# Performance work log

Measured on AMD Instinct MI355X. Metric: run time of the kernel, lower is better.

## Reference

```python
import jax, jax.numpy as jnp
import numpy as np
from jax import lax

HID, PROJ, DYN = 256, 256, 64
HW, BS, NQ = 6400, 16, 100


def setup_inputs() -> dict:
    key = jax.random.key(0)
    ks = jax.random.split(key, 10)
    p = lambda k, shape: jax.random.normal(k, shape, jnp.float32) * 0.02
    return {
        "query_feat": jax.random.normal(ks[0], (HW, BS, HID), jnp.float32),
        "support_feat": jax.random.normal(ks[1], (NQ, BS, HID), jnp.float32),
        "h": 80,
        "w": 80,
        "Wq": p(ks[2], (HID, PROJ)), "bq": jnp.zeros((PROJ,), jnp.float32),
        "Ws": p(ks[3], (HID, PROJ)), "bsp": jnp.zeros((PROJ,), jnp.float32),
        "W1": p(ks[4], (PROJ, DYN)), "b1": jnp.zeros((DYN,), jnp.float32),
        "W2": p(ks[5], (DYN, HID)), "b2": jnp.zeros((HID,), jnp.float32),
    }


def reference(query_feat, support_feat, h, w, Wq, bq, Ws, bsp, W1, b1, W2, b2):
    # query_feat: [hw, bs, c] -> [bs, hw, c]; support_feat: [nq, bs, c] -> [bs, nq, c]
    qf = jnp.transpose(query_feat, (1, 0, 2))
    sf = jnp.transpose(support_feat, (1, 0, 2))
    bsz, nq = sf.shape[0], sf.shape[1]
    hw = h * w

    fs_proj = sf @ Ws + bsp                      # [bs, nq, proj]
    fq_proj = qf @ Wq + bq                       # [bs, hw, proj]
    pattern = jnp.tanh(jax.nn.relu(fs_proj @ W1 + b1) @ W2 + b2)
    fs_feat = (pattern + 1.0) * fs_proj          # [bs, nq, proj]

    # bmm(fq, fs^T).T -> [bs, nq, hw]
    sim = jnp.einsum("bkp,bnp->bnk", fq_proj, fs_feat)
    similarity = sim.reshape(bsz, nq, h, w)

    # coordinate grid: x varies along w, y along h; flattened [hw, 2]
    gy = jnp.arange(h, dtype=jnp.float32) + 0.5
    gx = jnp.arange(w, dtype=jnp.float32) + 0.5
    X, Y = jnp.meshgrid(gx, gy, indexing="xy")  # each [h, w]
    coord = jnp.stack([X, Y], axis=-1).reshape(hw, 2)
    side = jnp.array([w, h], dtype=jnp.float32)

    sm = jax.nn.softmax(sim, axis=-1)            # [bs, nq, hw]
    proposal_for_loss = jnp.einsum("bnk,kd->bnd", sm, coord) / side

    # argmax peak -> one-hot -> 3x3 max-pool dilation (note (w,h) reshape per original)
    max_pos = jnp.argmax(sim, axis=-1)           # [bs, nq]
    max_mask = jax.nn.one_hot(max_pos, hw, dtype=jnp.float32).reshape(bsz, nq, w, h)
    local_mask = lax.reduce_window(
        max_mask, -jnp.inf, lax.max,
        window_dimensions=(1, 1, 3, 3), window_strides=(1, 1, 1, 1),
        padding=[(0, 0), (0, 0), (1, 1), (1, 1)],
    ).reshape(bsz, nq, hw)

    local_sm = sm * local_mask
    local_sm = local_sm / (jnp.sum(local_sm, axis=-1, keepdims=True) + 1e-10)
    proposals = jnp.einsum("bnk,kd->bnd", local_sm, coord) / side

    return proposal_for_loss, similarity, proposals
```

## Files before the change

### kernel.cpp

```cpp
#include <hip/hip_runtime.h>

#define HID 256
#define PROJ 256
#define DYN 64
#define HWD 6400
#define BSZ 16
#define NQ 100
#define HH 80
#define WW 80

typedef unsigned short u16;
typedef u16 u16x8 __attribute__((ext_vector_type(8)));
typedef __bf16 bf16x8 __attribute__((ext_vector_type(8)));
typedef float f32x4 __attribute__((ext_vector_type(4)));

__device__ __forceinline__ float bf2f(u16 h) {
    union { unsigned u; float f; } c; c.u = ((unsigned)h) << 16; return c.f;
}
__device__ __forceinline__ u16 f2bf(float f) {
    union { float f; unsigned u; } c; c.f = f;
    return (u16)((c.u + 0x7FFFu + ((c.u >> 16) & 1u)) >> 16);
}

__global__ __launch_bounds__(1024, 1) void kpre(
    const float* __restrict__ support,
    const float* __restrict__ Wq, const float* __restrict__ bq,
    const float* __restrict__ Ws, const float* __restrict__ bsp,
    const float* __restrict__ W1, const float* __restrict__ b1,
    const float* __restrict__ W2, const float* __restrict__ b2,
    u16* __restrict__ pack, float* __restrict__ cvec)
{
    const int c = blockIdx.x;
    const int b = blockIdx.y;
    const int t = threadIdx.x;

    __shared__ __align__(16) float sf_t[HID][8];
    __shared__ __align__(16) float part[4][8][256];
    __shared__ __align__(16) float fsp[8][PROJ];
    __shared__ __align__(16) float hidp[2][8][DYN];
    __shared__ __align__(16) float hid[8][DYN];
    __shared__ __align__(16) float fsf_t[PROJ][8];
    __shared__ float cacc[8][4];

    const int g = t >> 8;
    const int p = t & 255;

    {
        const int nl = t >> 7;
        const int i0 = (t & 127) * 2;
        const int n = c * 8 + nl;
        float v0 = 0.f, v1 = 0.f;
        if (n < NQ) {
            const float* sp = support + (size_t)n * (BSZ * HID) + (size_t)b * HID + i0;
            const float2 a = *reinterpret_cast<const float2*>(sp);
            v0 = a.x; v1 = a.y;
        }
        sf_t[i0][nl] = v0;
        sf_t[i0 + 1][nl] = v1;
    }
    __syncthreads();

    {
        float acc[8];
        #pragma unroll
        for (int n = 0; n < 8; ++n) acc[n] = 0.f;
        const int ibase = g * 64;
        float w[64];
        #pragma unroll
        for (int j = 0; j < 64; ++j)
            w[j] = Ws[(size_t)(ibase + j) * PROJ + p];
        __builtin_amdgcn_sched_barrier(0);
        #pragma unroll
        for (int j = 0; j < 64; ++j) {
            const f32x4 s0 = *reinterpret_cast<const f32x4*>(&sf_t[ibase + j][0]);
            const f32x4 s1 = *reinterpret_cast<const f32x4*>(&sf_t[ibase + j][4]);
            acc[0] += s0[0] * w[j]; acc[1] += s0[1] * w[j];
            acc[2] += s0[2] * w[j]; acc[3] += s0[3] * w[j];
            acc[4] += s1[0] * w[j]; acc[5] += s1[1] * w[j];
            acc[6] += s1[2] * w[j]; acc[7] += s1[3] * w[j];
        }
        #pragma unroll
        for (int n = 0; n < 8; ++n) part[g][n][p] = acc[n];
    }
    __syncthreads();
    {
        const int na = t >> 8;
        const float bb = bsp[p];
        #pragma unroll
        for (int k = 0; k < 2; ++k) {
            const int n = na + k * 4;
            fsp[n][p] = part[0][n][p] + part[1][n][p] + part[2][n][p] + part[3][n][p] + bb;
        }
    }
    __syncthreads();

    {
        const int ph = t >> 9;
        const int n = (t >> 6) & 7;
        const int d = t & 63;
        float a = 0.f;
        const int pb0 = ph * 128;
        #pragma unroll
        for (int pb = 0; pb < 128; pb += 64) {
            float w[64];
            #pragma unroll
            for (int j = 0; j < 64; ++j)
                w[j] = W1[(size_t)(pb0 + pb + j) * DYN + d];
            __builtin_amdgcn_sched_barrier(0);
            #pragma unroll
            for (int j = 0; j < 64; j += 4) {
                const f32x4 s = *reinterpret_cast<const f32x4*>(&fsp[n][pb0 + pb + j]);
                a += s[0] * w[j] + s[1] * w[j + 1] + s[2] * w[j + 2] + s[3] * w[j + 3];
            }
        }
        hidp[ph][n][d] = a;
    }
    __syncthreads();
    if (t < 512) {
        const int n = t >> 6, d = t & 63;
        const float a = hidp[0][n][d] + hidp[1][n][d] + b1[d];
        hid[n][d] = a > 0.f ? a : 0.f;
    }
    __syncthreads();

    {
        const int nh = t >> 8;
        const int n0 = nh * 2, n1 = nh * 2 + 1;
        const float bqv = bq[p];
        const float b2v = b2[p];
        float w[64];
        #pragma unroll
        for (int d = 0; d < 64; ++d) w[d] = W2[(size_t)d * PROJ + p];
        __builtin_amdgcn_sched_barrier(0);
        float a0 = 0.f, a1 = 0.f;
        #pragma unroll
        for (int d0 = 0; d0 < 64; d0 += 4) {
            const f32x4 h0 = *reinterpret_cast<const f32x4*>(&hid[n0][d0]);
            const f32x4 h1 = *reinterpret_cast<const f32x4*>(&hid[n1][d0]);
            a0 += h0[0] * w[d0] + h0[1] * w[d0 + 1] + h0[2] * w[d0 + 2] + h0[3] * w[d0 + 3];
            a1 += h1[0] * w[d0] + h1[1] * w[d0 + 1] + h1[2] * w[d0 + 2] + h1[3] * w[d0 + 3];
        }
        const float pat0 = tanhf(a0 + b2v);
        const float pat1 = tanhf(a1 + b2v);
        const float ff0 = (pat0 + 1.f) * fsp[n0][p];
        const float ff1 = (pat1 + 1.f) * fsp[n1][p];
        *reinterpret_cast<float2*>(&fsf_t[p][n0]) = make_float2(ff0, ff1);
        float cp0 = bqv * ff0, cp1 = bqv * ff1;
        for (int off = 32; off > 0; off >>= 1) {
            cp0 += __shfl_down(cp0, off);
            cp1 += __shfl_down(cp1, off);
        }
        const int lane = t & 63;
        const int ps = (t >> 6) & 3;
        if (lane == 0) { cacc[n0][ps] = cp0; cacc[n1][ps] = cp1; }
    }
    __syncthreads();
    if (t < 8) {
        const int n = c * 8 + t;
        if (n < NQ) cvec[b * NQ + n] = cacc[t][0] + cacc[t][1] + cacc[t][2] + cacc[t][3];
    }

    {
        const int h = p;
        float acc[8];
        #pragma unroll
        for (int n = 0; n < 8; ++n) acc[n] = 0.f;
        const int pbase = g * 64;
        f32x4 wv4[16];
        #pragma unroll
        for (int k = 0; k < 16; ++k)
            wv4[k] = *reinterpret_cast<const f32x4*>(Wq + (size_t)h * PROJ + pbase + k * 4);
        __builtin_amdgcn_sched_barrier(0);
        #pragma unroll
        for (int k = 0; k < 16; ++k) {
            #pragma unroll
            for (int m = 0; m < 4; ++m) {
                const int pp = pbase + k * 4 + m;
                const float w = wv4[k][m];
                const f32x4 f0 = *reinterpret_cast<const f32x4*>(&fsf_t[pp][0]);
                const f32x4 f1 = *reinterpret_cast<const f32x4*>(&fsf_t[pp][4]);
                acc[0] += f0[0] * w; acc[1] += f0[1] * w;
                acc[2] += f0[2] * w; acc[3] += f0[3] * w;
                acc[4] += f1[0] * w; acc[5] += f1[1] * w;
                acc[6] += f1[2] * w; acc[7] += f1[3] * w;
            }
        }
        #pragma unroll
        for (int n = 0; n < 8; ++n) part[g][n][h] = acc[n];
    }
    __syncthreads();

    {
        const int h = p;
        const int na = t >> 8;
        const int ks = h >> 5, quad = (h >> 3) & 3, j = h & 7;
        const int nt = c >> 1;
        #pragma unroll
        for (int k = 0; k < 2; ++k) {
            const int nl = na + k * 4;
            const int n = c * 8 + nl;
            float f = part[0][nl][h] + part[1][nl][h] + part[2][nl][h] + part[3][nl][h];
            if (n >= NQ) f = 0.f;
            const u16 hi = f2bf(f);
            const u16 lo = f2bf(f - bf2f(hi));
            const int nit = (c & 1) * 8 + nl;
            const int lane2 = quad * 16 + nit;
            const size_t base = ((((size_t)b * 2 + 0) * 8 + ks) * 8 + nt) * 512 + lane2 * 8 + j;
            pack[base] = hi;
            pack[base + (size_t)8 * 8 * 512] = lo;
        }
    }
}

__global__ __launch_bounds__(256, 3) void ksim(
    const float* __restrict__ qf,
    const u16* __restrict__ pack,
    const float* __restrict__ cvec,
    float* __restrict__ sim)
{
    const int mc = blockIdx.x;
    const int b  = blockIdx.y;
    const int wv = threadIdx.x >> 6;
    const int lane = threadIdx.x & 63;
    const int quad = lane >> 4, l16 = lane & 15;

    __shared__ __align__(16) u16 sbuf[2][14][512];

    const u16* pbase = pack + (size_t)b * (2 * 8 * 8 * 64 * 8);

    #define STAGE(KS, BUF)                                                          \
        do {                                                                        \
            for (int s14 = wv; s14 < 14; s14 += 4) {                                \
                const int s_ = s14 / 7, nt_ = s14 % 7;                              \
                const u16* g_ = pbase + ((size_t)(s_ * 8 + (KS)) * 8 + nt_) * 512   \
                                + (size_t)lane * 8;                                 \
                __builtin_amdgcn_global_load_lds(                                   \
                    (const __attribute__((address_space(1))) void*)g_,              \
                    (__attribute__((address_space(3))) void*)&sbuf[BUF][s14][0],    \
                    16, 0, 0);                                                      \
            }                                                                       \
        } while (0)

    f32x4 acc[7];
    #pragma unroll
    for (int nt = 0; nt < 7; ++nt) acc[nt] = (f32x4){0.f, 0.f, 0.f, 0.f};

    const int row = mc * 64 + wv * 16 + l16;
    const float* ap = qf + (size_t)row * (BSZ * HID) + b * HID + quad * 8;

    f32x4 af[16];
    {
        const float* p0 = ap + 0 * 32;
        const float* p1 = ap + 1 * 32;
        const float* p2 = ap + 2 * 32;
        const float* p3 = ap + 3 * 32;
        const float* p4 = ap + 4 * 32;
        const float* p5 = ap + 5 * 32;
        const float* p6 = ap + 6 * 32;
        const float* p7 = ap + 7 * 32;
        asm volatile(
            "global_load_dwordx4 %0, %16, off\n\t"
            "global_load_dwordx4 %1, %16, off offset:16\n\t"
            "global_load_dwordx4 %2, %17, off\n\t"
            "global_load_dwordx4 %3, %17, off offset:16\n\t"
            "global_load_dwordx4 %4, %18, off\n\t"
            "global_load_dwordx4 %5, %18, off offset:16\n\t"
            "global_load_dwordx4 %6, %19, off\n\t"
            "global_load_dwordx4 %7, %19, off offset:16\n\t"
            "global_load_dwordx4 %8, %20, off\n\t"
            "global_load_dwordx4 %9, %20, off offset:16\n\t"
            "global_load_dwordx4 %10, %21, off\n\t"
            "global_load_dwordx4 %11, %21, off offset:16\n\t"
            "global_load_dwordx4 %12, %22, off\n\t"
            "global_load_dwordx4 %13, %22, off offset:16\n\t"
            "global_load_dwordx4 %14, %23, off\n\t"
            "global_load_dwordx4 %15, %23, off offset:16\n\t"
            "s_waitcnt vmcnt(0)"
            : "=&v"(af[0]), "=&v"(af[1]), "=&v"(af[2]), "=&v"(af[3]),
              "=&v"(af[4]), "=&v"(af[5]), "=&v"(af[6]), "=&v"(af[7]),
              "=&v"(af[8]), "=&v"(af[9]), "=&v"(af[10]), "=&v"(af[11]),
              "=&v"(af[12]), "=&v"(af[13]), "=&v"(af[14]), "=&v"(af[15])
            : "v"(p0), "v"(p1), "v"(p2), "v"(p3),
              "v"(p4), "v"(p5), "v"(p6), "v"(p7));
    }

    STAGE(0, 0);

    bf16x8 Ahi[8], Alo[8];
    #pragma unroll
    for (int ks = 0; ks < 8; ++ks) {
        #pragma unroll
        for (int j = 0; j < 4; ++j) {
            const float v0 = af[2 * ks][j];
            const __bf16 h0 = (__bf16)v0;
            Ahi[ks][j] = h0; Alo[ks][j] = (__bf16)(v0 - (float)h0);
            const float v1 = af[2 * ks + 1][j];
            const __bf16 h1 = (__bf16)v1;
            Ahi[ks][4 + j] = h1; Alo[ks][4 + j] = (__bf16)(v1 - (float)h1);
        }
    }
    __syncthreads();

    int buf = 0;
    #pragma unroll
    for (int ks = 0; ks < 8; ++ks) {
        if (ks < 7) STAGE(ks + 1, buf ^ 1);

        u16x8 uh[7];
        #pragma unroll
        for (int nt = 0; nt < 7; ++nt)
            uh[nt] = *reinterpret_cast<const u16x8*>(&sbuf[buf][nt][lane * 8]);
        #pragma unroll
        for (int nt = 0; nt < 7; ++nt) {
            const bf16x8 bh = __builtin_bit_cast(bf16x8, uh[nt]);
            acc[nt] = __builtin_amdgcn_mfma_f32_16x16x32_bf16(Ahi[ks], bh, acc[nt], 0, 0, 0);
        }
        #pragma unroll
        for (int nt = 0; nt < 7; ++nt) {
            const bf16x8 bh = __builtin_bit_cast(bf16x8, uh[nt]);
            acc[nt] = __builtin_amdgcn_mfma_f32_16x16x32_bf16(Alo[ks], bh, acc[nt], 0, 0, 0);
        }

        u16x8 ul[7];
        #pragma unroll
        for (int nt = 0; nt < 7; ++nt)
            ul[nt] = *reinterpret_cast<const u16x8*>(&sbuf[buf][7 + nt][lane * 8]);
        #pragma unroll
        for (int nt = 0; nt < 7; ++nt) {
            const bf16x8 bl = __builtin_bit_cast(bf16x8, ul[nt]);
            acc[nt] = __builtin_amdgcn_mfma_f32_16x16x32_bf16(Ahi[ks], bl, acc[nt], 0, 0, 0);
        }

        __syncthreads();
        buf ^= 1;
    }
    #undef STAGE

    const int kbase = mc * 64 + wv * 16 + quad * 4;
    #pragma unroll
    for (int nt = 0; nt < 7; ++nt) {
        const int n = nt * 16 + l16;
        if (n >= NQ) continue;
        const float cadd = cvec[b * NQ + n];
        f32x4 o = acc[nt];
        o[0] += cadd; o[1] += cadd; o[2] += cadd; o[3] += cadd;
        *reinterpret_cast<f32x4*>(sim + (size_t)(b * NQ + n) * HWD + kbase) = o;
    }
}

__global__ __launch_bounds__(128, 2) void kfin(
    const float* __restrict__ sim,
    float* __restrict__ out)
{
    const int bn = blockIdx.x;
    const int w = threadIdx.x >> 6;
    const int lane = threadIdx.x & 63;
    const float* src = sim + (size_t)bn * HWD;

    __shared__ float redf[2][8];

    const int base = w ? 12 : 0;
    const int cnt  = w ? 13 : 12;

    f32x4 v[13];
    #pragma unroll
    for (int j = 0; j < 13; ++j)
        if (j < cnt)
            v[j] = *reinterpret_cast<const f32x4*>(src + (base + j) * 256 + lane * 4);
    __builtin_amdgcn_sched_barrier(0);

    float bv = -3.4e38f; int bi = 0x7FFFFFFF;
    #pragma unroll
    for (int j = 0; j < 13; ++j) {
        if (j < cnt) {
            #pragma unroll
            for (int k = 0; k < 4; ++k) {
                if (v[j][k] > bv) { bv = v[j][k]; bi = (base + j) * 256 + lane * 4 + k; }
            }
        }
    }
    #pragma unroll
    for (int m = 1; m < 64; m <<= 1) {
        const float ov = __shfl_xor(bv, m);
        const int oi = __shfl_xor(bi, m);
        if (ov > bv || (ov == bv && oi < bi)) { bv = ov; bi = oi; }
    }
    if (lane == 0) { redf[w][0] = bv; redf[w][1] = __int_as_float(bi); }
    __syncthreads();
    {
        const float v0 = redf[0][0], v1 = redf[1][0];
        const int i0 = __float_as_int(redf[0][1]), i1 = __float_as_int(redf[1][1]);
        if (v1 > v0 || (v1 == v0 && i1 < i0)) { bv = v1; bi = i1; }
        else { bv = v0; bi = i0; }
    }
    const int xc = bi % WW, yc = bi / WW;

    float s1 = 0.f, sx = 0.f, sy = 0.f;
    float wl = 0.f, wx = 0.f, wyv = 0.f;
    const int g0 = base * 256 + lane * 4;
    int x = g0 % WW, y = g0 / WW;
    #pragma unroll
    for (int j = 0; j < 13; ++j) {
        if (j < cnt) {
            #pragma unroll
            for (int k = 0; k < 4; ++k) {
                int xe = x + k, ye = y;
                if (xe >= WW) { xe -= WW; ye += 1; }
                const float e = __expf(v[j][k] - bv);
                const float fx = (float)xe + 0.5f;
                const float fy = (float)ye + 0.5f;
                s1 += e; sx += e * fx; sy += e * fy;
                const int dx = xe - xc, dy = ye - yc;
                const bool inw = (dx >= -1 && dx <= 1 && dy >= -1 && dy <= 1);
                const float ew = inw ? e : 0.f;
                wl += ew; wx += ew * fx; wyv += ew * fy;
            }
        }
        x += 16; y += 3;
        if (x >= WW) { x -= WW; y += 1; }
    }
    #pragma unroll
    for (int m = 1; m < 64; m <<= 1) {
        s1 += __shfl_xor(s1, m);
        sx += __shfl_xor(sx, m);
        sy += __shfl_xor(sy, m);
        wl += __shfl_xor(wl, m);
        wx += __shfl_xor(wx, m);
        wyv += __shfl_xor(wyv, m);
    }
    if (lane == 0) {
        redf[w][2] = s1; redf[w][3] = sx; redf[w][4] = sy;
        redf[w][5] = wl; redf[w][6] = wx; redf[w][7] = wyv;
    }
    __syncthreads();

    if (w == 0 && lane == 0) {
        const float S1 = redf[0][2] + redf[1][2];
        const float SX = redf[0][3] + redf[1][3];
        const float SY = redf[0][4] + redf[1][4];
        const float WL = redf[0][5] + redf[1][5];
        const float WX = redf[0][6] + redf[1][6];
        const float WY = redf[0][7] + redf[1][7];
        const float invS = 1.f / S1;
        out[(size_t)bn * 2 + 0] = SX * invS / (float)WW;
        out[(size_t)bn * 2 + 1] = SY * invS / (float)HH;
        const float den = WL + 1e-10f * S1;
        const size_t pbase = 3200 + (size_t)BSZ * NQ * HWD;
        out[pbase + (size_t)bn * 2 + 0] = WX / den / (float)WW;
        out[pbase + (size_t)bn * 2 + 1] = WY / den / (float)HH;
    }
}

extern "C" void kernel_launch(void* const* d_in, const int* in_sizes, int n_in,
                              void* d_out, int out_size, void* d_ws, size_t ws_size,
                              hipStream_t stream) {
    const float* qf  = (const float*)d_in[0];
    const float* sf  = (const float*)d_in[1];
    const float* Wq  = (const float*)d_in[4];
    const float* bq  = (const float*)d_in[5];
    const float* Ws  = (const float*)d_in[6];
    const float* bsp = (const float*)d_in[7];
    const float* W1  = (const float*)d_in[8];
    const float* b1  = (const float*)d_in[9];
    const float* W2  = (const float*)d_in[10];
    const float* b2  = (const float*)d_in[11];

    u16*   pack  = (u16*)d_ws;
    float* cvec  = (float*)((char*)d_ws + 2097152);
    float* out   = (float*)d_out;
    float* sim   = out + 3200;

    kpre<<<dim3(14, 16), 1024, 0, stream>>>(sf, Wq, bq, Ws, bsp, W1, b1, W2, b2, pack, cvec);
    ksim<<<dim3(100, 16), 256, 0, stream>>>(qf, pack, cvec, sim);
    kfin<<<1600, 64 * 2, 0, stream>>>(sim, out);
}
```

Measured before the change: 253.0 us.

## Replace LDS-staged B tiles with per-wave direct register loads and single-wave blocks

```diff
diff --git a/kernel.cpp b/kernel.cpp
--- a/kernel.cpp
+++ b/kernel.cpp
@@ -212,41 +212,24 @@
     }
 }
 
-__global__ __launch_bounds__(256, 3) void ksim(
+__global__ __launch_bounds__(64, 3) void ksim(
     const float* __restrict__ qf,
     const u16* __restrict__ pack,
     const float* __restrict__ cvec,
     float* __restrict__ sim)
 {
-    const int mc = blockIdx.x;
+    const int bx = blockIdx.x;
     const int b  = blockIdx.y;
-    const int wv = threadIdx.x >> 6;
-    const int lane = threadIdx.x & 63;
+    const int lane = threadIdx.x;
     const int quad = lane >> 4, l16 = lane & 15;
 
-    __shared__ __align__(16) u16 sbuf[2][14][512];
-
-    const u16* pbase = pack + (size_t)b * (2 * 8 * 8 * 64 * 8);
-
-    #define STAGE(KS, BUF)                                                          \
-        do {                                                                        \
-            for (int s14 = wv; s14 < 14; s14 += 4) {                                \
-                const int s_ = s14 / 7, nt_ = s14 % 7;                              \
-                const u16* g_ = pbase + ((size_t)(s_ * 8 + (KS)) * 8 + nt_) * 512   \
-                                + (size_t)lane * 8;                                 \
-                __builtin_amdgcn_global_load_lds(                                   \
-                    (const __attribute__((address_space(1))) void*)g_,              \
-                    (__attribute__((address_space(3))) void*)&sbuf[BUF][s14][0],    \
-                    16, 0, 0);                                                      \
-            }                                                                       \
-        } while (0)
-
     f32x4 acc[7];
     #pragma unroll
     for (int nt = 0; nt < 7; ++nt) acc[nt] = (f32x4){0.f, 0.f, 0.f, 0.f};
 
-    const int row = mc * 64 + wv * 16 + l16;
+    const int row = bx * 16 + l16;
     const float* ap = qf + (size_t)row * (BSZ * HID) + b * HID + quad * 8;
+    const u16* pb = pack + (size_t)b * 65536 + (size_t)lane * 8;
 
     f32x4 af[16];
     {
@@ -284,8 +267,6 @@
               "v"(p4), "v"(p5), "v"(p6), "v"(p7));
     }
 
-    STAGE(0, 0);
-
     bf16x8 Ahi[8], Alo[8];
     #pragma unroll
     for (int ks = 0; ks < 8; ++ks) {
@@ -299,44 +280,61 @@
             Ahi[ks][4 + j] = h1; Alo[ks][4 + j] = (__bf16)(v1 - (float)h1);
         }
     }
-    __syncthreads();
-
-    int buf = 0;
-    #pragma unroll
-    for (int ks = 0; ks < 8; ++ks) {
-        if (ks < 7) STAGE(ks + 1, buf ^ 1);
-
-        u16x8 uh[7];
-        #pragma unroll
-        for (int nt = 0; nt < 7; ++nt)
-            uh[nt] = *reinterpret_cast<const u16x8*>(&sbuf[buf][nt][lane * 8]);
-        #pragma unroll
-        for (int nt = 0; nt < 7; ++nt) {
-            const bf16x8 bh = __builtin_bit_cast(bf16x8, uh[nt]);
-            acc[nt] = __builtin_amdgcn_mfma_f32_16x16x32_bf16(Ahi[ks], bh, acc[nt], 0, 0, 0);
-        }
-        #pragma unroll
-        for (int nt = 0; nt < 7; ++nt) {
-            const bf16x8 bh = __builtin_bit_cast(bf16x8, uh[nt]);
-            acc[nt] = __builtin_amdgcn_mfma_f32_16x16x32_bf16(Alo[ks], bh, acc[nt], 0, 0, 0);
-        }
-
-        u16x8 ul[7];
-        #pragma unroll
-        for (int nt = 0; nt < 7; ++nt)
-            ul[nt] = *reinterpret_cast<const u16x8*>(&sbuf[buf][7 + nt][lane * 8]);
-        #pragma unroll
-        for (int nt = 0; nt < 7; ++nt) {
-            const bf16x8 bl = __builtin_bit_cast(bf16x8, ul[nt]);
-            acc[nt] = __builtin_amdgcn_mfma_f32_16x16x32_bf16(Ahi[ks], bl, acc[nt], 0, 0, 0);
-        }
-
-        __syncthreads();
-        buf ^= 1;
-    }
-    #undef STAGE
-
-    const int kbase = mc * 64 + wv * 16 + quad * 4;
+
+    #define ISSUE7(F, PA, PB)                                                   \
+        asm volatile(                                                           \
+            "global_load_dwordx4 %0, %7, off\n\t"                               \
+            "global_load_dwordx4 %1, %7, off offset:1024\n\t"                   \
+            "global_load_dwordx4 %2, %7, off offset:2048\n\t"                   \
+            "global_load_dwordx4 %3, %7, off offset:3072\n\t"                   \
+            "global_load_dwordx4 %4, %8, off\n\t"                               \
+            "global_load_dwordx4 %5, %8, off offset:1024\n\t"                   \
+            "global_load_dwordx4 %6, %8, off offset:2048"                       \
+            : "=&v"((F)[0]), "=&v"((F)[1]), "=&v"((F)[2]), "=&v"((F)[3]),       \
+              "=&v"((F)[4]), "=&v"((F)[5]), "=&v"((F)[6])                       \
+            : "v"(PA), "v"(PB))
+    #define WAIT7 do { asm volatile("s_waitcnt vmcnt(7)" ::: "memory");         \
+                       __builtin_amdgcn_sched_barrier(0); } while (0)
+
+    f32x4 fH[7], fL[7];
+
+    {
+        const u16* hA = pb;
+        ISSUE7(fH, hA, hA + 2048);
+    }
+
+    #define KS_BODY(KS)                                                          \
+    {                                                                            \
+        const u16* lA = pb + 32768 + (KS) * 4096;                                \
+        ISSUE7(fL, lA, lA + 2048);            \
+        WAIT7;                                                  \
+        _Pragma("unroll")                                                        \
+        for (int nt = 0; nt < 7; ++nt) {                                         \
+            const bf16x8 bh = __builtin_bit_cast(bf16x8, fH[nt]);                \
+            acc[nt] = __builtin_amdgcn_mfma_f32_16x16x32_bf16(Ahi[KS], bh, acc[nt], 0, 0, 0); \
+            acc[nt] = __builtin_amdgcn_mfma_f32_16x16x32_bf16(Alo[KS], bh, acc[nt], 0, 0, 0); \
+        }                                                                        \
+        const u16* hA = pb + ((KS) + 1) * 4096;       \
+        ISSUE7(fH, hA, hA + 2048);             \
+        WAIT7;                                                  \
+        _Pragma("unroll")                                                        \
+        for (int nt = 0; nt < 7; ++nt) {                                         \
+            const bf16x8 bl = __builtin_bit_cast(bf16x8, fL[nt]);                \
+            acc[nt] = __builtin_amdgcn_mfma_f32_16x16x32_bf16(Ahi[KS], bl, acc[nt], 0, 0, 0); \
+        }                                                                        \
+    }
+
+    KS_BODY(0) KS_BODY(1) KS_BODY(2) KS_BODY(3)
+    KS_BODY(4) KS_BODY(5) KS_BODY(6) KS_BODY(7)
+
+    #undef KS_BODY
+    #undef WAIT7
+    #undef ISSUE7
+
+    asm volatile("s_waitcnt vmcnt(0)" ::: "memory");
+    __builtin_amdgcn_sched_barrier(0);
+
+    const int kbase = bx * 16 + quad * 4;
     #pragma unroll
     for (int nt = 0; nt < 7; ++nt) {
         const int n = nt * 16 + l16;
@@ -471,6 +469,6 @@
     float* sim   = out + 3200;
 
     kpre<<<dim3(14, 16), 1024, 0, stream>>>(sf, Wq, bq, Ws, bsp, W1, b1, W2, b2, pack, cvec);
-    ksim<<<dim3(100, 16), 256, 0, stream>>>(qf, pack, cvec, sim);
+    ksim<<<dim3(400, 16), 64, 0, stream>>>(qf, pack, cvec, sim);
     kfin<<<1600, 64 * 2, 0, stream>>>(sim, out);
 }
```

New measurement: 264.9 us. 4.7% more time.

## Triple-buffer support tiles in ksim with prefetch distance two and explicit vmcnt waits

Applied to the files above, without the earlier changes.

```diff
diff --git a/kernel.cpp b/kernel.cpp
--- a/kernel.cpp
+++ b/kernel.cpp
@@ -224,19 +224,21 @@
     const int lane = threadIdx.x & 63;
     const int quad = lane >> 4, l16 = lane & 15;
 
-    __shared__ __align__(16) u16 sbuf[2][14][512];
-
-    const u16* pbase = pack + (size_t)b * (2 * 8 * 8 * 64 * 8);
-
-    #define STAGE(KS, BUF)                                                          \
+    __shared__ __align__(16) u16 sbuf[3][16][512];
+
+    const u16* pbase = pack + (size_t)b * 65536;
+
+    #define STAGE(KS, SLOT)                                                         \
         do {                                                                        \
-            for (int s14 = wv; s14 < 14; s14 += 4) {                                \
-                const int s_ = s14 / 7, nt_ = s14 % 7;                              \
+            _Pragma("unroll")                                                       \
+            for (int i = 0; i < 4; ++i) {                                           \
+                const int s14 = wv * 4 + i;                                         \
+                const int s_ = s14 >> 3, nt_ = s14 & 7;                             \
                 const u16* g_ = pbase + ((size_t)(s_ * 8 + (KS)) * 8 + nt_) * 512   \
                                 + (size_t)lane * 8;                                 \
                 __builtin_amdgcn_global_load_lds(                                   \
                     (const __attribute__((address_space(1))) void*)g_,              \
-                    (__attribute__((address_space(3))) void*)&sbuf[BUF][s14][0],    \
+                    (__attribute__((address_space(3))) void*)&sbuf[SLOT][s14][0],   \
                     16, 0, 0);                                                      \
             }                                                                       \
         } while (0)
@@ -283,8 +285,8 @@
             : "v"(p0), "v"(p1), "v"(p2), "v"(p3),
               "v"(p4), "v"(p5), "v"(p6), "v"(p7));
     }
-
     STAGE(0, 0);
+    STAGE(1, 1);
 
     bf16x8 Ahi[8], Alo[8];
     #pragma unroll
@@ -301,39 +303,49 @@
     }
     __syncthreads();
 
-    int buf = 0;
-    #pragma unroll
-    for (int ks = 0; ks < 8; ++ks) {
-        if (ks < 7) STAGE(ks + 1, buf ^ 1);
-
-        u16x8 uh[7];
-        #pragma unroll
-        for (int nt = 0; nt < 7; ++nt)
-            uh[nt] = *reinterpret_cast<const u16x8*>(&sbuf[buf][nt][lane * 8]);
-        #pragma unroll
-        for (int nt = 0; nt < 7; ++nt) {
-            const bf16x8 bh = __builtin_bit_cast(bf16x8, uh[nt]);
-            acc[nt] = __builtin_amdgcn_mfma_f32_16x16x32_bf16(Ahi[ks], bh, acc[nt], 0, 0, 0);
-        }
-        #pragma unroll
-        for (int nt = 0; nt < 7; ++nt) {
-            const bf16x8 bh = __builtin_bit_cast(bf16x8, uh[nt]);
-            acc[nt] = __builtin_amdgcn_mfma_f32_16x16x32_bf16(Alo[ks], bh, acc[nt], 0, 0, 0);
-        }
-
-        u16x8 ul[7];
-        #pragma unroll
-        for (int nt = 0; nt < 7; ++nt)
-            ul[nt] = *reinterpret_cast<const u16x8*>(&sbuf[buf][7 + nt][lane * 8]);
-        #pragma unroll
-        for (int nt = 0; nt < 7; ++nt) {
-            const bf16x8 bl = __builtin_bit_cast(bf16x8, ul[nt]);
-            acc[nt] = __builtin_amdgcn_mfma_f32_16x16x32_bf16(Ahi[ks], bl, acc[nt], 0, 0, 0);
-        }
-
-        __syncthreads();
-        buf ^= 1;
-    }
+    #define WAITBAR(N)                                                              \
+        do {                                                                        \
+            asm volatile("s_waitcnt vmcnt(" #N ")" ::: "memory");                   \
+            __builtin_amdgcn_sched_barrier(0);                                      \
+            __builtin_amdgcn_s_barrier();                                           \
+            __builtin_amdgcn_sched_barrier(0);                                      \
+        } while (0)
+
+    #define KS_BODY(KS, SR, SW, DOSTAGE)                                             \
+    {                                                                                \
+        if (DOSTAGE) STAGE((KS) + 2, SW);                                            \
+        u16x8 uh[7];                                                                 \
+        _Pragma("unroll")                                                            \
+        for (int nt = 0; nt < 7; ++nt)                                               \
+            uh[nt] = *reinterpret_cast<const u16x8*>(&sbuf[SR][nt][lane * 8]);       \
+        _Pragma("unroll")                                                            \
+        for (int nt = 0; nt < 7; ++nt) {                                             \
+            const bf16x8 bh = __builtin_bit_cast(bf16x8, uh[nt]);                    \
+            acc[nt] = __builtin_amdgcn_mfma_f32_16x16x32_bf16(Ahi[KS], bh, acc[nt], 0, 0, 0); \
+            acc[nt] = __builtin_amdgcn_mfma_f32_16x16x32_bf16(Alo[KS], bh, acc[nt], 0, 0, 0); \
+        }                                                                            \
+        u16x8 ul[7];                                                                 \
+        _Pragma("unroll")                                                            \
+        for (int nt = 0; nt < 7; ++nt)                                               \
+            ul[nt] = *reinterpret_cast<const u16x8*>(&sbuf[SR][8 + nt][lane * 8]);   \
+        _Pragma("unroll")                                                            \
+        for (int nt = 0; nt < 7; ++nt) {                                             \
+            const bf16x8 bl = __builtin_bit_cast(bf16x8, ul[nt]);                    \
+            acc[nt] = __builtin_amdgcn_mfma_f32_16x16x32_bf16(Ahi[KS], bl, acc[nt], 0, 0, 0); \
+        }                                                                            \
+    }
+
+    KS_BODY(0, 0, 2, 1) WAITBAR(4);
+    KS_BODY(1, 1, 0, 1) WAITBAR(4);
+    KS_BODY(2, 2, 1, 1) WAITBAR(4);
+    KS_BODY(3, 0, 2, 1) WAITBAR(4);
+    KS_BODY(4, 1, 0, 1) WAITBAR(4);
+    KS_BODY(5, 2, 1, 1) WAITBAR(4);
+    KS_BODY(6, 0, 2, 0) WAITBAR(0);
+    KS_BODY(7, 1, 0, 0)
+
+    #undef KS_BODY
+    #undef WAITBAR
     #undef STAGE
 
     const int kbase = mc * 64 + wv * 16 + quad * 4;
```

Result: no change. 250.2 us (-1.1%).
